# Kernel tuning notes

Hardware: AMD Instinct MI355X
Metric: run time of the kernel (lower is better)

Reference implementation:

```python
import jax, jax.numpy as jnp
import numpy as np

SH_DEGREE = 1
D_SH = (SH_DEGREE + 1) ** 2  # 4
SCALE_MIN = 0.5
SCALE_MAX = 15.0
MULTIPLIER = 0.1
EPS = 1e-8


def quat_to_rotmat(q):
    # q: [..., 4] (w, x, y, z), assumed (near-)normalized
    w, x, y, z = q[..., 0], q[..., 1], q[..., 2], q[..., 3]
    return jnp.stack([
        jnp.stack([1 - 2 * (y * y + z * z), 2 * (x * y - w * z), 2 * (x * z + w * y)], -1),
        jnp.stack([2 * (x * y + w * z), 1 - 2 * (x * x + z * z), 2 * (y * z - w * x)], -1),
        jnp.stack([2 * (x * z - w * y), 2 * (y * z + w * x), 1 - 2 * (x * x + y * y)], -1),
    ], -2)


def setup_inputs() -> dict:
    key = jax.random.key(0)
    ks = jax.random.split(key, 6)
    B, N = 8, 131072
    H, W = 256, 512
    # valid SE(3) extrinsics (rotation from random unit quaternion)
    q = jax.random.normal(ks[0], (B, 1, 4), dtype=jnp.float32)
    q = q / jnp.linalg.norm(q, axis=-1, keepdims=True)
    R = quat_to_rotmat(q)
    t = jax.random.normal(ks[1], (B, 1, 3), dtype=jnp.float32)
    ext = jnp.zeros((B, 1, 4, 4), jnp.float32)
    ext = ext.at[..., :3, :3].set(R).at[..., :3, 3].set(t).at[..., 3, 3].set(1.0)
    # normalized pinhole intrinsics
    K = jnp.array([[1.2, 0.0, 0.5], [0.0, 1.2, 0.5], [0.0, 0.0, 1.0]], jnp.float32)
    K = jnp.broadcast_to(K, (B, 1, 3, 3))
    coordinates = jax.random.uniform(ks[2], (B, N, 2), dtype=jnp.float32)
    depths = jax.random.uniform(ks[3], (B, N), dtype=jnp.float32, minval=0.5, maxval=10.0)
    opacities = jax.random.uniform(ks[4], (B, N), dtype=jnp.float32)
    raw_gaussians = jax.random.normal(ks[5], (B, N, 7 + 3 * D_SH), dtype=jnp.float32)
    return {"extrinsics": ext, "intrinsics": K, "coordinates": coordinates,
            "depths": depths, "opacities": opacities, "raw_gaussians": raw_gaussians,
            "h": H, "w": W}


def reference(extrinsics, intrinsics, coordinates, depths, opacities, raw_gaussians, h, w):
    # sh mask: degree-0 untouched, degree d scaled by 0.1 * 0.25**d
    sh_mask = jnp.ones((D_SH,), jnp.float32)
    for d in range(1, SH_DEGREE + 1):
        sh_mask = sh_mask.at[d ** 2:(d + 1) ** 2].set(0.1 * 0.25 ** d)

    scales_raw = raw_gaussians[..., :3]
    rot_raw = raw_gaussians[..., 3:7]
    sh = raw_gaussians[..., 7:]

    scales = SCALE_MIN + (SCALE_MAX - SCALE_MIN) * jax.nn.sigmoid(scales_raw)

    # scale multiplier from inverse of 2x2 top-left of intrinsics
    pixel_size = 1.0 / jnp.array([w, h], jnp.float32)
    a = intrinsics[..., 0, 0]; b = intrinsics[..., 0, 1]
    c = intrinsics[..., 1, 0]; d = intrinsics[..., 1, 1]
    det = a * d - b * c
    inv2 = jnp.stack([jnp.stack([d, -b], -1), jnp.stack([-c, a], -1)], -2) / det[..., None, None]
    multiplier = (MULTIPLIER * jnp.einsum('...ij,j->...i', inv2, pixel_size)).sum(-1)  # [B,1]

    scales = scales * depths[..., None] * multiplier[..., None]  # [B,N,3]

    rotations = rot_raw / (jnp.linalg.norm(rot_raw, axis=-1, keepdims=True) + EPS)  # [B,N,4]

    sh = sh.reshape(*sh.shape[:-1], 3, D_SH) * sh_mask  # [B,N,3,D_SH]

    # covariance = R diag(s^2) R^T, then rotate into world frame
    R = quat_to_rotmat(rotations)  # [B,N,3,3]
    cov = jnp.einsum('...ij,...j,...kj->...ik', R, scales * scales, R)
    c2w = extrinsics[..., :3, :3]  # [B,1,3,3]
    cov = jnp.einsum('...ij,...jk,...lk->...il', c2w, cov, c2w)  # [B,N,3,3]

    # world rays: unproject pixel coords with depth 1, normalize, rotate to world
    coords_h = jnp.concatenate([coordinates, jnp.ones_like(coordinates[..., :1])], -1)  # [B,N,3]
    Kinv = jnp.linalg.inv(intrinsics)  # [B,1,3,3]
    dirs = jnp.einsum('...ij,...j->...i', Kinv, coords_h)
    dirs = dirs / jnp.linalg.norm(dirs, axis=-1, keepdims=True)
    dirs_w = jnp.einsum('...ij,...j->...i', c2w, dirs)  # [B,N,3]
    origins = jnp.broadcast_to(extrinsics[..., :3, 3], dirs_w.shape)
    means = origins + dirs_w * depths[..., None]  # [B,N,3]

    # rotate SH: l=0 identity; l=1 Wigner-D equals c2w in the (y,z,x) permuted basis
    p = jnp.array([1, 2, 0])
    D1 = c2w[..., p, :][..., :, p]  # [B,1,3,3]
    sh0 = sh[..., :1]
    sh1 = jnp.einsum('...ij,...cj->...ci', D1, sh[..., 1:4])
    harmonics = jnp.concatenate([sh0, sh1], -1)  # [B,N,3,D_SH]

    rotations_b = jnp.broadcast_to(rotations, (*scales.shape[:-1], 4))
    return (means, cov, harmonics, opacities, scales, rotations_b)
```

## Files before the change

kernel.cpp:

```cpp
#include <hip/hip_runtime.h>
#include <math.h>

#define SCALE_MIN 0.5f
#define SCALE_MAX 15.0f
#define MULTIPLIER 0.1f
#define EPS 1e-8f

typedef float v4f __attribute__((ext_vector_type(4)));
typedef float v2f __attribute__((ext_vector_type(2)));


#define G 256

#define L_MEAN  0
#define L_COV   768
#define L_HARM  3072
#define L_SCALE 6144
#define L_TOT   6912

__global__ __launch_bounds__(256) void mono_gaussian_adapter_kernel(
    const float* __restrict__ ext,
    const float* __restrict__ intr,
    const float* __restrict__ coord,
    const float* __restrict__ depth,
    const float* __restrict__ opac,
    const float* __restrict__ rawg,
    const int* __restrict__ hp,
    const int* __restrict__ wp,
    float* __restrict__ out,
    int bpb,
    int BN)
{
    __shared__ float lds[L_TOT];

    const int tid = threadIdx.x;
    const int blk = blockIdx.x;
    const int gid = blk * G + tid;
    const int b = blk / bpb;

    {
        const v4f* gin = (const v4f*)(rawg + (long long)blk * (G * 19));
        v4f* l4 = (v4f*)lds;
        #pragma unroll
        for (int i = 0; i < 4; ++i) {
            int idx = tid + i * 256;
            l4[idx] = __builtin_nontemporal_load(gin + idx);
        }
        {
            int idx = tid + 4 * 256;
            if (idx < (G * 19 / 4))
                l4[idx] = __builtin_nontemporal_load(gin + idx);
        }
    }

    float inv_w = 1.0f / (float)wp[0];
    float inv_h = 1.0f / (float)hp[0];

    const float* E = ext + b * 16;
    float c00=E[0],  c01=E[1],  c02=E[2],  t0=E[3];
    float c10=E[4],  c11=E[5],  c12=E[6],  t1=E[7];
    float c20=E[8],  c21=E[9],  c22=E[10], t2=E[11];

    const float* Kb = intr + b * 9;
    float k00=Kb[0],k01=Kb[1],k02=Kb[2];
    float k10=Kb[3],k11=Kb[4],k12=Kb[5];
    float k20=Kb[6],k21=Kb[7],k22=Kb[8];

    float det2 = k00*k11 - k01*k10;
    float mult = MULTIPLIER * ((k11*inv_w - k01*inv_h) + (k00*inv_h - k10*inv_w)) / det2;

    float det3 = k00*(k11*k22 - k12*k21)
               + k01*(k12*k20 - k10*k22)
               + k02*(k10*k21 - k11*k20);
    float id3 = 1.0f / det3;
    float i00 = (k11*k22 - k12*k21)*id3;
    float i01 = (k02*k21 - k01*k22)*id3;
    float i02 = (k01*k12 - k02*k11)*id3;
    float i10 = (k12*k20 - k10*k22)*id3;
    float i11 = (k00*k22 - k02*k20)*id3;
    float i12 = (k02*k10 - k00*k12)*id3;
    float i20 = (k10*k21 - k11*k20)*id3;
    float i21 = (k01*k20 - k00*k21)*id3;
    float i22 = (k00*k11 - k01*k10)*id3;

    v2f uv = __builtin_nontemporal_load((const v2f*)coord + gid);
    float dep = __builtin_nontemporal_load(depth + gid);
    float op  = __builtin_nontemporal_load(opac + gid);

    __syncthreads();

    const float* g = lds + tid * 19;
    float sr0 = g[0], sr1 = g[1], sr2 = g[2];
    float q0 = g[3], q1 = g[4], q2 = g[5], q3 = g[6];
    float sh00=g[7],  sh01=g[8],  sh02=g[9],  sh03=g[10];
    float sh10=g[11], sh11=g[12], sh12=g[13], sh13=g[14];
    float sh20=g[15], sh21=g[16], sh22=g[17], sh23=g[18];

    __syncthreads();

    float s0 = SCALE_MIN + (SCALE_MAX - SCALE_MIN) / (1.0f + __expf(-sr0));
    float s1 = SCALE_MIN + (SCALE_MAX - SCALE_MIN) / (1.0f + __expf(-sr1));
    float s2 = SCALE_MIN + (SCALE_MAX - SCALE_MIN) / (1.0f + __expf(-sr2));
    float dm = dep * mult;
    s0 *= dm; s1 *= dm; s2 *= dm;

    float qn = sqrtf(q0*q0 + q1*q1 + q2*q2 + q3*q3) + EPS;
    float qi = 1.0f / qn;
    float qw = q0*qi, qx = q1*qi, qy = q2*qi, qz = q3*qi;

    float r00 = 1.0f - 2.0f*(qy*qy + qz*qz);
    float r01 = 2.0f*(qx*qy - qw*qz);
    float r02 = 2.0f*(qx*qz + qw*qy);
    float r10 = 2.0f*(qx*qy + qw*qz);
    float r11 = 1.0f - 2.0f*(qx*qx + qz*qz);
    float r12 = 2.0f*(qy*qz - qw*qx);
    float r20 = 2.0f*(qx*qz - qw*qy);
    float r21 = 2.0f*(qy*qz + qw*qx);
    float r22 = 1.0f - 2.0f*(qx*qx + qy*qy);

    float v0 = s0*s0, v1 = s1*s1, v2 = s2*s2;
    float p00 = r00*r00*v0 + r01*r01*v1 + r02*r02*v2;
    float p01 = r00*r10*v0 + r01*r11*v1 + r02*r12*v2;
    float p02 = r00*r20*v0 + r01*r21*v1 + r02*r22*v2;
    float p11 = r10*r10*v0 + r11*r11*v1 + r12*r12*v2;
    float p12 = r10*r20*v0 + r11*r21*v1 + r12*r22*v2;
    float p22 = r20*r20*v0 + r21*r21*v1 + r22*r22*v2;

    float m00 = c00*p00 + c01*p01 + c02*p02;
    float m01 = c00*p01 + c01*p11 + c02*p12;
    float m02 = c00*p02 + c01*p12 + c02*p22;
    float m10 = c10*p00 + c11*p01 + c12*p02;
    float m11 = c10*p01 + c11*p11 + c12*p12;
    float m12 = c10*p02 + c11*p12 + c12*p22;
    float m20 = c20*p00 + c21*p01 + c22*p02;
    float m21 = c20*p01 + c21*p11 + c22*p12;
    float m22 = c20*p02 + c21*p12 + c22*p22;

    float q00 = m00*c00 + m01*c01 + m02*c02;
    float q01 = m00*c10 + m01*c11 + m02*c12;
    float q02 = m00*c20 + m01*c21 + m02*c22;
    float q11 = m10*c10 + m11*c11 + m12*c12;
    float q12 = m10*c20 + m11*c21 + m12*c22;
    float q22 = m20*c20 + m21*c21 + m22*c22;

    float d0 = i00*uv.x + i01*uv.y + i02;
    float d1 = i10*uv.x + i11*uv.y + i12;
    float d2 = i20*uv.x + i21*uv.y + i22;
    float rn = rsqrtf(d0*d0 + d1*d1 + d2*d2);
    d0 *= rn; d1 *= rn; d2 *= rn;
    float w0 = c00*d0 + c01*d1 + c02*d2;
    float w1 = c10*d0 + c11*d1 + c12*d2;
    float w2 = c20*d0 + c21*d1 + c22*d2;
    float me0 = t0 + w0*dep;
    float me1 = t1 + w1*dep;
    float me2 = t2 + w2*dep;

    float D00=c11, D01=c12, D02=c10;
    float D10=c21, D11=c22, D12=c20;
    float D20=c01, D21=c02, D22=c00;
    const float msk = 0.1f * 0.25f;
    float a1 = msk*sh01, a2 = msk*sh02, a3 = msk*sh03;
    float b1 = msk*sh11, b2 = msk*sh12, b3 = msk*sh13;
    float e1 = msk*sh21, e2 = msk*sh22, e3 = msk*sh23;
    v4f h0 = { sh00, D00*a1 + D01*a2 + D02*a3,
                     D10*a1 + D11*a2 + D12*a3,
                     D20*a1 + D21*a2 + D22*a3 };
    v4f h1 = { sh10, D00*b1 + D01*b2 + D02*b3,
                     D10*b1 + D11*b2 + D12*b3,
                     D20*b1 + D21*b2 + D22*b3 };
    v4f h2 = { sh20, D00*e1 + D01*e2 + D02*e3,
                     D10*e1 + D11*e2 + D12*e3,
                     D20*e1 + D21*e2 + D22*e3 };

    __builtin_nontemporal_store(op, out + 24*BN + gid);
    v4f rq = { qw, qx, qy, qz };
    __builtin_nontemporal_store(rq, (v4f*)(out + 28LL*BN) + gid);

    {
        float* lm = lds + L_MEAN + tid * 3;
        lm[0] = me0; lm[1] = me1; lm[2] = me2;

        float* lc = lds + L_COV + tid * 9;
        lc[0]=q00; lc[1]=q01; lc[2]=q02;
        lc[3]=q01; lc[4]=q11; lc[5]=q12;
        lc[6]=q02; lc[7]=q12; lc[8]=q22;

        v4f* lh = (v4f*)(lds + L_HARM + tid * 12);
        lh[0] = h0; lh[1] = h1; lh[2] = h2;

        float* ls = lds + L_SCALE + tid * 3;
        ls[0] = s0; ls[1] = s1; ls[2] = s2;
    }
    __syncthreads();

    {
        const v4f* l4 = (const v4f*)lds;
        v4f* gm = (v4f*)(out + (long long)blk * (3 * G));
        v4f* gs = (v4f*)(out + 25LL * BN + (long long)blk * (3 * G));
        if (tid < 192) {
            __builtin_nontemporal_store(l4[(L_MEAN / 4) + tid], gm + tid);
            __builtin_nontemporal_store(l4[(L_SCALE / 4) + tid], gs + tid);
        }
        v4f* gc = (v4f*)(out + 3LL * BN + (long long)blk * (9 * G));
        #pragma unroll
        for (int i = 0; i < 2; ++i) {
            int idx = tid + i * 256;
            __builtin_nontemporal_store(l4[(L_COV / 4) + idx], gc + idx);
        }
        {   int idx = tid + 512;
            if (idx < 576)
                __builtin_nontemporal_store(l4[(L_COV / 4) + idx], gc + idx);
        }
        v4f* gh = (v4f*)(out + 12LL * BN + (long long)blk * (12 * G));
        #pragma unroll
        for (int i = 0; i < 3; ++i) {
            int idx = tid + i * 256;
            __builtin_nontemporal_store(l4[(L_HARM / 4) + idx], gh + idx);
        }
    }
}

extern "C" void kernel_launch(void* const* d_in, const int* in_sizes, int n_in,
                              void* d_out, int out_size, void* d_ws, size_t ws_size,
                              hipStream_t stream) {
    const float* ext   = (const float*)d_in[0];
    const float* intr  = (const float*)d_in[1];
    const float* coord = (const float*)d_in[2];
    const float* depth = (const float*)d_in[3];
    const float* opac  = (const float*)d_in[4];
    const float* rawg  = (const float*)d_in[5];
    const int*   hp    = (const int*)d_in[6];
    const int*   wp    = (const int*)d_in[7];

    int BN = in_sizes[3];
    int B  = in_sizes[0] / 16;
    int N  = BN / B;
    int blocks = BN / 256;
    int bpb = N / 256;

    mono_gaussian_adapter_kernel<<<blocks, 256, 0, stream>>>(
        ext, intr, coord, depth, opac, rawg, hp, wp,
        (float*)d_out, bpb, BN);
}
```

Before: 212.5 us.

## Stage per-wavefront through LDS with direct global-to-LDS loads, drop block barriers

Each wavefront now owns a private LDS slice. Its 64 raw Gaussian records are loaded straight into LDS with global_load_lds, followed by a vmcnt wait instead of __syncthreads. The output staging reuses that same slice in two phases (mean/cov/scale, then harmonics), which shrinks LDS per block and, together with the launch bound hint, allows more resident blocks. The opacity and rotation stores are moved earlier. The intent is to remove block-wide barriers and the register round-trip for loads and to raise memory-level parallelism. It relies on in-order LDS access within a wave for correctness.

```diff
diff --git a/kernel.cpp b/kernel.cpp
--- a/kernel.cpp
+++ b/kernel.cpp
@@ -10,15 +10,12 @@
 typedef float v2f __attribute__((ext_vector_type(2)));
 
 
-#define G 256
-
-#define L_MEAN  0
-#define L_COV   768
-#define L_HARM  3072
-#define L_SCALE 6144
-#define L_TOT   6912
-
-__global__ __launch_bounds__(256) void mono_gaussian_adapter_kernel(
+#define WVF 1216
+#define A_MEAN  0
+#define A_COV   192
+#define A_SCALE 768
+
+__global__ __launch_bounds__(256, 8) void mono_gaussian_adapter_kernel(
     const float* __restrict__ ext,
     const float* __restrict__ intr,
     const float* __restrict__ coord,
@@ -31,27 +28,38 @@
     int bpb,
     int BN)
 {
-    __shared__ float lds[L_TOT];
-
-    const int tid = threadIdx.x;
-    const int blk = blockIdx.x;
-    const int gid = blk * G + tid;
-    const int b = blk / bpb;
-
-    {
-        const v4f* gin = (const v4f*)(rawg + (long long)blk * (G * 19));
-        v4f* l4 = (v4f*)lds;
+    __shared__ __align__(16) float lds[4 * WVF];
+
+    const int tid  = threadIdx.x;
+    const int lane = tid & 63;
+    const int wid  = tid >> 6;
+    const int blk  = blockIdx.x;
+    const int gid  = blk * 256 + tid;
+    const int gw   = blk * 4 + wid;
+    const int b    = blk / bpb;
+
+    float* lw = lds + wid * WVF;
+
+    {
+        const v4f* gsrc = (const v4f*)(rawg + (long long)gw * (64 * 19));
         #pragma unroll
         for (int i = 0; i < 4; ++i) {
-            int idx = tid + i * 256;
-            l4[idx] = __builtin_nontemporal_load(gin + idx);
+            __builtin_amdgcn_global_load_lds(
+                (const __attribute__((address_space(1))) void*)(gsrc + i * 64 + lane),
+                (__attribute__((address_space(3))) void*)((v4f*)lw + i * 64),
+                16, 0, 0);
         }
-        {
-            int idx = tid + 4 * 256;
-            if (idx < (G * 19 / 4))
-                l4[idx] = __builtin_nontemporal_load(gin + idx);
+        if (lane < 48) {
+            __builtin_amdgcn_global_load_lds(
+                (const __attribute__((address_space(1))) void*)(gsrc + 256 + lane),
+                (__attribute__((address_space(3))) void*)((v4f*)lw + 256),
+                16, 0, 0);
         }
     }
+
+    v2f uv  = __builtin_nontemporal_load((const v2f*)coord + gid);
+    float dep = __builtin_nontemporal_load(depth + gid);
+    float op  = __builtin_nontemporal_load(opac + gid);
 
     float inv_w = 1.0f / (float)wp[0];
     float inv_h = 1.0f / (float)hp[0];
@@ -83,21 +91,15 @@
     float i21 = (k01*k20 - k00*k21)*id3;
     float i22 = (k00*k11 - k01*k10)*id3;
 
-    v2f uv = __builtin_nontemporal_load((const v2f*)coord + gid);
-    float dep = __builtin_nontemporal_load(depth + gid);
-    float op  = __builtin_nontemporal_load(opac + gid);
-
-    __syncthreads();
-
-    const float* g = lds + tid * 19;
+    asm volatile("s_waitcnt vmcnt(0)" ::: "memory");
+
+    const float* g = lw + lane * 19;
     float sr0 = g[0], sr1 = g[1], sr2 = g[2];
     float q0 = g[3], q1 = g[4], q2 = g[5], q3 = g[6];
     float sh00=g[7],  sh01=g[8],  sh02=g[9],  sh03=g[10];
     float sh10=g[11], sh11=g[12], sh12=g[13], sh13=g[14];
     float sh20=g[15], sh21=g[16], sh22=g[17], sh23=g[18];
 
-    __syncthreads();
-
     float s0 = SCALE_MIN + (SCALE_MAX - SCALE_MIN) / (1.0f + __expf(-sr0));
     float s1 = SCALE_MIN + (SCALE_MAX - SCALE_MIN) / (1.0f + __expf(-sr1));
     float s2 = SCALE_MIN + (SCALE_MAX - SCALE_MIN) / (1.0f + __expf(-sr2));
@@ -107,6 +109,10 @@
     float qn = sqrtf(q0*q0 + q1*q1 + q2*q2 + q3*q3) + EPS;
     float qi = 1.0f / qn;
     float qw = q0*qi, qx = q1*qi, qy = q2*qi, qz = q3*qi;
+
+    __builtin_nontemporal_store(op, out + 24LL*BN + gid);
+    v4f rq = { qw, qx, qy, qz };
+    __builtin_nontemporal_store(rq, (v4f*)(out + 28LL*BN) + gid);
 
     float r00 = 1.0f - 2.0f*(qy*qy + qz*qz);
     float r01 = 2.0f*(qx*qy - qw*qz);
@@ -172,51 +178,44 @@
                      D10*e1 + D11*e2 + D12*e3,
                      D20*e1 + D21*e2 + D22*e3 };
 
-    __builtin_nontemporal_store(op, out + 24*BN + gid);
-    v4f rq = { qw, qx, qy, qz };
-    __builtin_nontemporal_store(rq, (v4f*)(out + 28LL*BN) + gid);
-
-    {
-        float* lm = lds + L_MEAN + tid * 3;
+    {
+        float* lm = lw + A_MEAN + lane * 3;
         lm[0] = me0; lm[1] = me1; lm[2] = me2;
 
-        float* lc = lds + L_COV + tid * 9;
+        float* lc = lw + A_COV + lane * 9;
         lc[0]=q00; lc[1]=q01; lc[2]=q02;
         lc[3]=q01; lc[4]=q11; lc[5]=q12;
         lc[6]=q02; lc[7]=q12; lc[8]=q22;
 
-        v4f* lh = (v4f*)(lds + L_HARM + tid * 12);
+        float* ls = lw + A_SCALE + lane * 3;
+        ls[0] = s0; ls[1] = s1; ls[2] = s2;
+    }
+    {
+        const v4f* l4 = (const v4f*)lw;
+        v4f* gm = (v4f*)(out + (long long)gw * 192);
+        v4f* gs = (v4f*)(out + 25LL*BN + (long long)gw * 192);
+        if (lane < 48) {
+            __builtin_nontemporal_store(l4[(A_MEAN / 4) + lane], gm + lane);
+            __builtin_nontemporal_store(l4[(A_SCALE / 4) + lane], gs + lane);
+        }
+        v4f* gc = (v4f*)(out + 3LL*BN + (long long)gw * 576);
+        #pragma unroll
+        for (int i = 0; i < 2; ++i)
+            __builtin_nontemporal_store(l4[(A_COV / 4) + lane + i*64], gc + lane + i*64);
+        if (lane < 16)
+            __builtin_nontemporal_store(l4[(A_COV / 4) + lane + 128], gc + lane + 128);
+    }
+
+    {
+        v4f* lh = (v4f*)lw + lane * 3;
         lh[0] = h0; lh[1] = h1; lh[2] = h2;
-
-        float* ls = lds + L_SCALE + tid * 3;
-        ls[0] = s0; ls[1] = s1; ls[2] = s2;
-    }
-    __syncthreads();
-
-    {
-        const v4f* l4 = (const v4f*)lds;
-        v4f* gm = (v4f*)(out + (long long)blk * (3 * G));
-        v4f* gs = (v4f*)(out + 25LL * BN + (long long)blk * (3 * G));
-        if (tid < 192) {
-            __builtin_nontemporal_store(l4[(L_MEAN / 4) + tid], gm + tid);
-            __builtin_nontemporal_store(l4[(L_SCALE / 4) + tid], gs + tid);
-        }
-        v4f* gc = (v4f*)(out + 3LL * BN + (long long)blk * (9 * G));
+    }
+    {
+        const v4f* l4 = (const v4f*)lw;
+        v4f* gh = (v4f*)(out + 12LL*BN + (long long)gw * 768);
         #pragma unroll
-        for (int i = 0; i < 2; ++i) {
-            int idx = tid + i * 256;
-            __builtin_nontemporal_store(l4[(L_COV / 4) + idx], gc + idx);
-        }
-        {   int idx = tid + 512;
-            if (idx < 576)
-                __builtin_nontemporal_store(l4[(L_COV / 4) + idx], gc + idx);
-        }
-        v4f* gh = (v4f*)(out + 12LL * BN + (long long)blk * (12 * G));
-        #pragma unroll
-        for (int i = 0; i < 3; ++i) {
-            int idx = tid + i * 256;
-            __builtin_nontemporal_store(l4[(L_HARM / 4) + idx], gh + idx);
-        }
+        for (int i = 0; i < 3; ++i)
+            __builtin_nontemporal_store(l4[lane + i*64], gh + lane + i*64);
     }
 }
 
```

Result: slower. 217.6 us (+2.4%).
